# Optimization experiments

Measured on AMD Instinct MI355X. Metric: run time of the kernel, lower is better.

Reference implementation:

```python
import jax, jax.numpy as jnp
import numpy as np

E = 8        # num experts
K = 2        # top-k
H = 1024     # hidden size
F = 3584     # intermediate (ffn) size
B, S = 1, 2048


def setup_inputs() -> dict:
    key = jax.random.key(0)
    ks = jax.random.split(key, 5)
    scale_h = 1.0 / np.sqrt(H)
    scale_f = 1.0 / np.sqrt(F)
    return {
        "hidden_states": jax.random.normal(ks[0], (B, S, H), jnp.float32),
        "gate_w": jax.random.normal(ks[1], (E, H), jnp.float32) * scale_h,  # Linear [out,in]
        "w1": jax.random.normal(ks[2], (E, F, H), jnp.float32) * scale_h,
        "w3": jax.random.normal(ks[3], (E, F, H), jnp.float32) * scale_h,
        "w2": jax.random.normal(ks[4], (E, H, F), jnp.float32) * scale_f,
    }


def reference(hidden_states, gate_w, w1, w3, w2):
    b, s, h = hidden_states.shape
    x = hidden_states.reshape(-1, h)                       # [T,H]
    T = x.shape[0]
    # Router: softmax over experts, top-k, renormalize
    router_logits = x @ gate_w.T                           # [T,E]
    routing_weights = jax.nn.softmax(router_logits.astype(jnp.float32), axis=-1)
    topk_w, topk_idx = jax.lax.top_k(routing_weights, K)   # [T,K]
    topk_w = topk_w / jnp.sum(topk_w, axis=-1, keepdims=True)
    # Per-token, per-expert combine weight (0 for unselected experts) --
    # matches the original mask-and-sum over all experts.
    tok = jnp.arange(T)
    expert_weights = jnp.zeros((T, E), jnp.float32).at[tok[:, None], topk_idx].add(topk_w)  # [T,E]
    # Dense per-expert SiLU-gated MLP over all tokens (as the reference loop does),
    # vectorized across experts.
    g = jnp.einsum("th,efh->etf", x, w1)                   # [E,T,F]
    u = jnp.einsum("th,efh->etf", x, w3)                   # [E,T,F]
    act = jax.nn.silu(g) * u                               # [E,T,F]
    y = jnp.einsum("etf,ehf->eth", act, w2)                # [E,T,H]
    out = jnp.einsum("eth,te->th", y, expert_weights.astype(y.dtype))  # [T,H]
    return out.reshape(b, s, h)
```

## Files before the change

kernel.cpp:

```cpp
#include <hip/hip_runtime.h>
#include <hip/hip_bf16.h>

#define T_TOK 2048
#define HID   1024
#define FF    3584
#define NE    8
#define TOPK  2
#define GRIDY 24

typedef __bf16 bf16x8 __attribute__((ext_vector_type(8)));
typedef float  f32x4  __attribute__((ext_vector_type(4)));
typedef unsigned short u16x8 __attribute__((ext_vector_type(8)));

#define WS_COUNTS   0u
#define WS_OFFSETS  64u
#define WS_TILECNT  128u
#define WS_TLE      256u
#define WS_TLM      512u
#define WS_TOPKI    4096u
#define WS_TOPKW    20480u
#define WS_SLOTPOS  36864u
#define WS_SLOTROW  53248u
#define WS_ROUTETOK 69632u
#define WS_XG       131072u
#define WS_ACT      (WS_XG + 4096u*1024u*2u)
#define WS_Y        (WS_ACT + 4096u*3584u*2u)
#define Y_STRIDE    (4096u*1024u)

static __device__ __forceinline__ unsigned short f2bf(float f) {
    unsigned int u = __builtin_bit_cast(unsigned int, f);
    u += 0x7FFFu + ((u >> 16) & 1u);
    return (unsigned short)(u >> 16);
}
static __device__ __forceinline__ unsigned int cvtpk(float lo, float hi) {
    unsigned int r;
    asm("v_cvt_pk_bf16_f32 %0, %1, %2" : "=v"(r) : "v"(lo), "v"(hi));
    return r;
}

__global__ __launch_bounds__(256) void k_router(
    const float* __restrict__ x, const float* __restrict__ gw,
    int* __restrict__ counts, int* __restrict__ topki,
    float* __restrict__ topkw, int* __restrict__ slotpos)
{
    int t = blockIdx.x * 4 + (threadIdx.x >> 6);
    int l = threadIdx.x & 63;
    const float* xr = x + (size_t)t * HID;
    float acc[NE];
#pragma unroll
    for (int e = 0; e < NE; ++e) acc[e] = 0.f;
#pragma unroll
    for (int i = 0; i < 4; ++i) {
        int h = l * 4 + i * 256;
        float4 xv = *(const float4*)(xr + h);
#pragma unroll
        for (int e = 0; e < NE; ++e) {
            float4 g = *(const float4*)(gw + e * HID + h);
            acc[e] += xv.x * g.x + xv.y * g.y + xv.z * g.z + xv.w * g.w;
        }
    }
#pragma unroll
    for (int e = 0; e < NE; ++e) {
#pragma unroll
        for (int off = 32; off; off >>= 1) acc[e] += __shfl_xor(acc[e], off);
    }
    if (l == 0) {
        float best = -1e30f, second = -1e30f;
        int bi = 0, si = 0;
#pragma unroll
        for (int e = 0; e < NE; ++e) {
            float v = acc[e];
            if (v > best) { second = best; si = bi; best = v; bi = e; }
            else if (v > second) { second = v; si = e; }
        }
        float w0 = 1.f / (1.f + __expf(second - best));
        float w1 = 1.f - w0;
        topki[2 * t] = bi;  topki[2 * t + 1] = si;
        topkw[2 * t] = w0;  topkw[2 * t + 1] = w1;
        slotpos[2 * t]     = atomicAdd(&counts[bi], 1);
        slotpos[2 * t + 1] = atomicAdd(&counts[si], 1);
    }
}

__global__ void k_prefix(const int* __restrict__ counts, int* __restrict__ offsets,
                         int* __restrict__ tle, int* __restrict__ tlm,
                         int* __restrict__ tilecnt) {
    if (threadIdx.x == 0) {
        int o = 0;
#pragma unroll
        for (int e = 0; e < NE; ++e) { offsets[e] = o; o += counts[e]; }
        int n = 0;
        for (int e = 0; e < NE; ++e) {
            int t = (counts[e] + 255) >> 8;
            for (int i = 0; i < t; ++i) { tle[n] = e; tlm[n] = i; ++n; }
        }
        tilecnt[0] = n;
    }
}

__global__ void k_fill(const int* __restrict__ topki, const int* __restrict__ slotpos,
                       const int* __restrict__ offsets, int* __restrict__ routetok,
                       int* __restrict__ slotrow) {
    int j = blockIdx.x * blockDim.x + threadIdx.x;
    if (j >= T_TOK * TOPK) return;
    int e = topki[j];
    int row = offsets[e] + slotpos[j];
    routetok[row] = j >> 1;
    slotrow[j] = row;
}

__global__ void k_gather(const float* __restrict__ x, const int* __restrict__ routetok,
                         unsigned short* __restrict__ xg) {
    int j = blockIdx.x * blockDim.x + threadIdx.x;
    int r = j >> 8;
    int c = (j & 255) * 4;
    int tok = routetok[r];
    float4 v = *(const float4*)(x + (size_t)tok * HID + c);
    ushort4 o;
    o.x = f2bf(v.x); o.y = f2bf(v.y); o.z = f2bf(v.z); o.w = f2bf(v.w);
    int sc = c ^ ((r & 7) << 3);
    *(ushort4*)(xg + (size_t)r * HID + sc) = o;
}

__global__ __launch_bounds__(512, 4) void k_gemm1(
    const unsigned short* __restrict__ xg, const float* __restrict__ w1,
    const float* __restrict__ w3, const int* __restrict__ counts,
    const int* __restrict__ offsets, const int* __restrict__ tle,
    const int* __restrict__ tlm, const int* __restrict__ tilecnt,
    unsigned short* __restrict__ act)
{
    int by = blockIdx.y;
    if (by >= tilecnt[0]) return;
    int e = tle[by];
    int rbase = tlm[by] * 256;
    int cnt = counts[e], obase = offsets[e];
    int fbase = blockIdx.x * 64;

    __shared__ __align__(16) unsigned short lA[256 * 64];
    __shared__ __align__(16) unsigned short lB1[64 * 64];
    __shared__ __align__(16) unsigned short lB3[64 * 64];

    int tid = threadIdx.x;
    const int ra0 = tid >> 3, ca = (tid & 7) * 8;
    const int rb0 = tid >> 4, cb = (tid & 15) * 4;
    const unsigned short* pa[4];
#pragma unroll
    for (int i = 0; i < 4; ++i) {
        int r = obase + rbase + ra0 + 64 * i;
        if (r > 4095) r = 4095;
        pa[i] = xg + (size_t)r * HID + ca;
    }
    const float* w1e = w1 + ((size_t)e * FF + fbase) * HID;
    const float* w3e = w3 + ((size_t)e * FF + fbase) * HID;
    const float* pb1[2];
    const float* pb3[2];
    int wba[2];
#pragma unroll
    for (int i = 0; i < 2; ++i) {
        int row = rb0 + 32 * i;
        pb1[i] = w1e + (size_t)row * HID + cb;
        pb3[i] = w3e + (size_t)row * HID + cb;
        wba[i] = row * 64 + (cb ^ ((row & 7) << 3));
    }

    int lane = tid & 63, wv = tid >> 6, wr = wv >> 1, wc = wv & 1;
    int klane = (lane >> 4) * 8;
    int swzA = (((obase & 7) + (lane & 7)) & 7) << 3;
    int swzB = (lane & 7) << 3;
    f32x4 accg[4][2], accu[4][2];
#pragma unroll
    for (int m = 0; m < 4; ++m)
#pragma unroll
        for (int n = 0; n < 2; ++n) {
            accg[m][n] = (f32x4){0.f, 0.f, 0.f, 0.f};
            accu[m][n] = (f32x4){0.f, 0.f, 0.f, 0.f};
        }

    u16x8 ra[4]; float4 r1[2], r3[2];
#pragma unroll
    for (int i = 0; i < 4; ++i) ra[i] = *(const u16x8*)(pa[i]);
#pragma unroll
    for (int i = 0; i < 2; ++i) { r1[i] = *(const float4*)(pb1[i]); r3[i] = *(const float4*)(pb3[i]); }

    for (int kt = 0; kt < HID / 64; ++kt) {
#pragma unroll
        for (int i = 0; i < 4; ++i)
            *(u16x8*)(lA + (ra0 + 64 * i) * 64 + ca) = ra[i];
#pragma unroll
        for (int i = 0; i < 2; ++i) {
            uint2 p;
            p.x = cvtpk(r1[i].x, r1[i].y); p.y = cvtpk(r1[i].z, r1[i].w);
            *(uint2*)(lB1 + wba[i]) = p;
            p.x = cvtpk(r3[i].x, r3[i].y); p.y = cvtpk(r3[i].z, r3[i].w);
            *(uint2*)(lB3 + wba[i]) = p;
        }
        __syncthreads();
        if (kt < HID / 64 - 1) {
            int kof = (kt + 1) * 64;
#pragma unroll
            for (int i = 0; i < 4; ++i) ra[i] = *(const u16x8*)(pa[i] + kof);
#pragma unroll
            for (int i = 0; i < 2; ++i) {
                r1[i] = *(const float4*)(pb1[i] + kof);
                r3[i] = *(const float4*)(pb3[i] + kof);
            }
        }
#pragma unroll
        for (int kk = 0; kk < 64; kk += 32) {
            int kc = kk + klane;
            int kA = kc ^ swzA, kB = kc ^ swzB;
            bf16x8 a[4], b1[2], b3[2];
#pragma unroll
            for (int m = 0; m < 4; ++m)
                a[m] = *(const bf16x8*)(lA + (wr * 64 + m * 16 + (lane & 15)) * 64 + kA);
#pragma unroll
            for (int n = 0; n < 2; ++n) {
                b1[n] = *(const bf16x8*)(lB1 + (wc * 32 + n * 16 + (lane & 15)) * 64 + kB);
                b3[n] = *(const bf16x8*)(lB3 + (wc * 32 + n * 16 + (lane & 15)) * 64 + kB);
            }
#pragma unroll
            for (int m = 0; m < 4; ++m)
#pragma unroll
                for (int n = 0; n < 2; ++n) {
                    accg[m][n] = __builtin_amdgcn_mfma_f32_16x16x32_bf16(a[m], b1[n], accg[m][n], 0, 0, 0);
                    accu[m][n] = __builtin_amdgcn_mfma_f32_16x16x32_bf16(a[m], b3[n], accu[m][n], 0, 0, 0);
                }
        }
        __syncthreads();
    }

#pragma unroll
    for (int m = 0; m < 4; ++m)
#pragma unroll
        for (int n = 0; n < 2; ++n)
#pragma unroll
            for (int r = 0; r < 4; ++r) {
                int lr = wr * 64 + m * 16 + (lane >> 4) * 4 + r;
                if (rbase + lr < cnt) {
                    float g = accg[m][n][r], u = accu[m][n][r];
                    float s = g / (1.f + __expf(-g));
                    int row = obase + rbase + lr;
                    int col = fbase + wc * 32 + n * 16 + (lane & 15);
                    int scol = col ^ ((row & 7) << 3);
                    act[(size_t)row * FF + scol] = f2bf(s * u);
                }
            }
}

__global__ __launch_bounds__(512, 4) void k_gemm2(
    const unsigned short* __restrict__ act, const float* __restrict__ w2,
    const int* __restrict__ counts, const int* __restrict__ offsets,
    const int* __restrict__ tle, const int* __restrict__ tlm,
    const int* __restrict__ tilecnt, float* __restrict__ y, int ks)
{
    int by = blockIdx.y;
    if (by >= tilecnt[0]) return;
    int e = tle[by];
    int rbase = tlm[by] * 256;
    int cnt = counts[e], obase = offsets[e];
    int hbase = blockIdx.x * 128;
    int z = blockIdx.z;
    const int KTOT = FF / 64;
    int per = (KTOT + ks - 1) / ks;
    int kt0 = z * per;
    int ktn = (KTOT < kt0 + per ? KTOT : kt0 + per) - kt0;
    int kb0 = kt0 * 64;

    __shared__ __align__(16) unsigned short lA[256 * 64];
    __shared__ __align__(16) unsigned short lB[128 * 64];

    int tid = threadIdx.x;
    const int ra0 = tid >> 3, ca = (tid & 7) * 8;
    const unsigned short* pa[4];
#pragma unroll
    for (int i = 0; i < 4; ++i) {
        int r = obase + rbase + ra0 + 64 * i;
        if (r > 4095) r = 4095;
        pa[i] = act + (size_t)r * FF + kb0 + ca;
    }
    int hr = tid >> 2, cbf = (tid & 3) * 16;
    const float* pb = w2 + ((size_t)e * HID + hbase + hr) * FF + kb0 + cbf;
    int wbb[2];
#pragma unroll
    for (int g = 0; g < 2; ++g)
        wbb[g] = hr * 64 + ((cbf + g * 8) ^ ((hr & 7) << 3));

    int lane = tid & 63, wv = tid >> 6;
    int wr = wv & 3, wc = wv >> 2;
    int klane = (lane >> 4) * 8;
    int swzA = (((obase & 7) + (lane & 7)) & 7) << 3;
    int swzB = (lane & 7) << 3;
    f32x4 acc[4][4];
#pragma unroll
    for (int m = 0; m < 4; ++m)
#pragma unroll
        for (int n = 0; n < 4; ++n) acc[m][n] = (f32x4){0.f, 0.f, 0.f, 0.f};

    u16x8 ra[4]; float4 rw[4];
#pragma unroll
    for (int i = 0; i < 4; ++i) ra[i] = *(const u16x8*)(pa[i]);
#pragma unroll
    for (int j = 0; j < 4; ++j) rw[j] = *(const float4*)(pb + 4 * j);

    for (int kt = 0; kt < ktn; ++kt) {
#pragma unroll
        for (int i = 0; i < 4; ++i)
            *(u16x8*)(lA + (ra0 + 64 * i) * 64 + ca) = ra[i];
#pragma unroll
        for (int g = 0; g < 2; ++g) {
            uint4 q;
            q.x = cvtpk(rw[2 * g].x, rw[2 * g].y);
            q.y = cvtpk(rw[2 * g].z, rw[2 * g].w);
            q.z = cvtpk(rw[2 * g + 1].x, rw[2 * g + 1].y);
            q.w = cvtpk(rw[2 * g + 1].z, rw[2 * g + 1].w);
            *(uint4*)(lB + wbb[g]) = q;
        }
        __syncthreads();
        if (kt < ktn - 1) {
            int kof = (kt + 1) * 64;
#pragma unroll
            for (int i = 0; i < 4; ++i) ra[i] = *(const u16x8*)(pa[i] + kof);
#pragma unroll
            for (int j = 0; j < 4; ++j) rw[j] = *(const float4*)(pb + kof + 4 * j);
        }
#pragma unroll
        for (int kk = 0; kk < 64; kk += 32) {
            int kc = kk + klane;
            int kA = kc ^ swzA, kB = kc ^ swzB;
            bf16x8 a[4], b[4];
#pragma unroll
            for (int m = 0; m < 4; ++m)
                a[m] = *(const bf16x8*)(lA + (wr * 64 + m * 16 + (lane & 15)) * 64 + kA);
#pragma unroll
            for (int n = 0; n < 4; ++n)
                b[n] = *(const bf16x8*)(lB + (wc * 64 + n * 16 + (lane & 15)) * 64 + kB);
#pragma unroll
            for (int m = 0; m < 4; ++m)
#pragma unroll
                for (int n = 0; n < 4; ++n)
                    acc[m][n] = __builtin_amdgcn_mfma_f32_16x16x32_bf16(a[m], b[n], acc[m][n], 0, 0, 0);
        }
        __syncthreads();
    }

    float* yz = y + (size_t)z * Y_STRIDE;
#pragma unroll
    for (int m = 0; m < 4; ++m)
#pragma unroll
        for (int n = 0; n < 4; ++n)
#pragma unroll
            for (int r = 0; r < 4; ++r) {
                int lr = wr * 64 + m * 16 + (lane >> 4) * 4 + r;
                if (rbase + lr < cnt) {
                    int col = hbase + wc * 64 + n * 16 + (lane & 15);
                    yz[(size_t)(obase + rbase + lr) * HID + col] = acc[m][n][r];
                }
            }
}

__global__ void k_combine(const float* __restrict__ y, const int* __restrict__ slotrow,
                          const float* __restrict__ topkw, float* __restrict__ out, int ks) {
    int j = blockIdx.x * blockDim.x + threadIdx.x;
    int t = j >> 8, c = j & 255;
    int r0 = slotrow[2 * t], r1 = slotrow[2 * t + 1];
    float w0 = topkw[2 * t], w1 = topkw[2 * t + 1];
    float4 a = {0.f, 0.f, 0.f, 0.f}, b = {0.f, 0.f, 0.f, 0.f};
    for (int z = 0; z < ks; ++z) {
        const float4* yz = (const float4*)(y + (size_t)z * Y_STRIDE);
        float4 av = yz[(size_t)r0 * 256 + c];
        float4 bv = yz[(size_t)r1 * 256 + c];
        a.x += av.x; a.y += av.y; a.z += av.z; a.w += av.w;
        b.x += bv.x; b.y += bv.y; b.z += bv.z; b.w += bv.w;
    }
    float4 o;
    o.x = w0 * a.x + w1 * b.x;
    o.y = w0 * a.y + w1 * b.y;
    o.z = w0 * a.z + w1 * b.z;
    o.w = w0 * a.w + w1 * b.w;
    ((float4*)out)[j] = o;
}

extern "C" void kernel_launch(void* const* d_in, const int* in_sizes, int n_in,
                              void* d_out, int out_size, void* d_ws, size_t ws_size,
                              hipStream_t stream) {
    const float* x  = (const float*)d_in[0];
    const float* gw = (const float*)d_in[1];
    const float* w1 = (const float*)d_in[2];
    const float* w3 = (const float*)d_in[3];
    const float* w2 = (const float*)d_in[4];
    float* out = (float*)d_out;

    char* ws = (char*)d_ws;
    int*   counts   = (int*)(ws + WS_COUNTS);
    int*   offsets  = (int*)(ws + WS_OFFSETS);
    int*   tilecnt  = (int*)(ws + WS_TILECNT);
    int*   tle      = (int*)(ws + WS_TLE);
    int*   tlm      = (int*)(ws + WS_TLM);
    int*   topki    = (int*)(ws + WS_TOPKI);
    float* topkw    = (float*)(ws + WS_TOPKW);
    int*   slotpos  = (int*)(ws + WS_SLOTPOS);
    int*   slotrow  = (int*)(ws + WS_SLOTROW);
    int*   routetok = (int*)(ws + WS_ROUTETOK);
    unsigned short* xg   = (unsigned short*)(ws + WS_XG);
    unsigned short* actb = (unsigned short*)(ws + WS_ACT);
    float* yb = (float*)(ws + WS_Y);

    size_t ybytes = (size_t)Y_STRIDE * 4;
    int ks = (ws_size >= (size_t)WS_Y + 3 * ybytes) ? 3 : 2;

    hipMemsetAsync(counts, 0, 64, stream);
    k_router<<<T_TOK / 4, 256, 0, stream>>>(x, gw, counts, topki, topkw, slotpos);
    k_prefix<<<1, 64, 0, stream>>>(counts, offsets, tle, tlm, tilecnt);
    k_fill<<<16, 256, 0, stream>>>(topki, slotpos, offsets, routetok, slotrow);
    k_gather<<<4096, 256, 0, stream>>>(x, routetok, xg);
    k_gemm1<<<dim3(FF / 64, GRIDY, 1), 512, 0, stream>>>(xg, w1, w3, counts, offsets, tle, tlm, tilecnt, actb);
    k_gemm2<<<dim3(HID / 128, GRIDY, ks), 512, 0, stream>>>(actb, w2, counts, offsets, tle, tlm, tilecnt, yb, ks);
    k_combine<<<2048, 256, 0, stream>>>(yb, slotrow, topkw, out, ks);
}
```

Before: 264.4 us.

## Enlarge gemm1 row tile to 512 tokens with 1024-thread blocks

```diff
diff --git a/kernel.cpp b/kernel.cpp
--- a/kernel.cpp
+++ b/kernel.cpp
@@ -6,7 +6,8 @@
 #define FF    3584
 #define NE    8
 #define TOPK  2
-#define GRIDY 24
+#define GRIDY1 16
+#define GRIDY2 24
 
 typedef __bf16 bf16x8 __attribute__((ext_vector_type(8)));
 typedef float  f32x4  __attribute__((ext_vector_type(4)));
@@ -15,8 +16,10 @@
 #define WS_COUNTS   0u
 #define WS_OFFSETS  64u
 #define WS_TILECNT  128u
-#define WS_TLE      256u
-#define WS_TLM      512u
+#define WS_TLE1     256u
+#define WS_TLM1     512u
+#define WS_TLE2     768u
+#define WS_TLM2     1024u
 #define WS_TOPKI    4096u
 #define WS_TOPKW    20480u
 #define WS_SLOTPOS  36864u
@@ -83,18 +86,21 @@
 }
 
 __global__ void k_prefix(const int* __restrict__ counts, int* __restrict__ offsets,
-                         int* __restrict__ tle, int* __restrict__ tlm,
+                         int* __restrict__ tl1e, int* __restrict__ tl1m,
+                         int* __restrict__ tl2e, int* __restrict__ tl2m,
                          int* __restrict__ tilecnt) {
     if (threadIdx.x == 0) {
         int o = 0;
 #pragma unroll
         for (int e = 0; e < NE; ++e) { offsets[e] = o; o += counts[e]; }
-        int n = 0;
+        int n1 = 0, n2 = 0;
         for (int e = 0; e < NE; ++e) {
-            int t = (counts[e] + 255) >> 8;
-            for (int i = 0; i < t; ++i) { tle[n] = e; tlm[n] = i; ++n; }
-        }
-        tilecnt[0] = n;
+            int t1 = (counts[e] + 511) >> 9;
+            for (int i = 0; i < t1; ++i) { tl1e[n1] = e; tl1m[n1] = i; ++n1; }
+            int t2 = (counts[e] + 255) >> 8;
+            for (int i = 0; i < t2; ++i) { tl2e[n2] = e; tl2m[n2] = i; ++n2; }
+        }
+        tilecnt[0] = n1; tilecnt[1] = n2;
     }
 }
 
@@ -122,7 +128,7 @@
     *(ushort4*)(xg + (size_t)r * HID + sc) = o;
 }
 
-__global__ __launch_bounds__(512, 4) void k_gemm1(
+__global__ __launch_bounds__(1024, 2) void k_gemm1(
     const unsigned short* __restrict__ xg, const float* __restrict__ w1,
     const float* __restrict__ w3, const int* __restrict__ counts,
     const int* __restrict__ offsets, const int* __restrict__ tle,
@@ -132,11 +138,11 @@
     int by = blockIdx.y;
     if (by >= tilecnt[0]) return;
     int e = tle[by];
-    int rbase = tlm[by] * 256;
+    int rbase = tlm[by] * 512;
     int cnt = counts[e], obase = offsets[e];
     int fbase = blockIdx.x * 64;
 
-    __shared__ __align__(16) unsigned short lA[256 * 64];
+    __shared__ __align__(16) unsigned short lA[512 * 64];
     __shared__ __align__(16) unsigned short lB1[64 * 64];
     __shared__ __align__(16) unsigned short lB3[64 * 64];
 
@@ -146,24 +152,16 @@
     const unsigned short* pa[4];
 #pragma unroll
     for (int i = 0; i < 4; ++i) {
-        int r = obase + rbase + ra0 + 64 * i;
+        int r = obase + rbase + ra0 + 128 * i;
         if (r > 4095) r = 4095;
         pa[i] = xg + (size_t)r * HID + ca;
     }
-    const float* w1e = w1 + ((size_t)e * FF + fbase) * HID;
-    const float* w3e = w3 + ((size_t)e * FF + fbase) * HID;
-    const float* pb1[2];
-    const float* pb3[2];
-    int wba[2];
-#pragma unroll
-    for (int i = 0; i < 2; ++i) {
-        int row = rb0 + 32 * i;
-        pb1[i] = w1e + (size_t)row * HID + cb;
-        pb3[i] = w3e + (size_t)row * HID + cb;
-        wba[i] = row * 64 + (cb ^ ((row & 7) << 3));
-    }
-
-    int lane = tid & 63, wv = tid >> 6, wr = wv >> 1, wc = wv & 1;
+    const float* pb1 = w1 + ((size_t)e * FF + fbase + rb0) * HID + cb;
+    const float* pb3 = w3 + ((size_t)e * FF + fbase + rb0) * HID + cb;
+    int wba = rb0 * 64 + (cb ^ ((rb0 & 7) << 3));
+
+    int lane = tid & 63, wv = tid >> 6;
+    int wr = wv >> 1, wc = wv & 1;
     int klane = (lane >> 4) * 8;
     int swzA = (((obase & 7) + (lane & 7)) & 7) << 3;
     int swzB = (lane & 7) << 3;
@@ -176,34 +174,30 @@
             accu[m][n] = (f32x4){0.f, 0.f, 0.f, 0.f};
         }
 
-    u16x8 ra[4]; float4 r1[2], r3[2];
+    u16x8 ra[4]; float4 r1, r3;
 #pragma unroll
     for (int i = 0; i < 4; ++i) ra[i] = *(const u16x8*)(pa[i]);
-#pragma unroll
-    for (int i = 0; i < 2; ++i) { r1[i] = *(const float4*)(pb1[i]); r3[i] = *(const float4*)(pb3[i]); }
+    r1 = *(const float4*)(pb1);
+    r3 = *(const float4*)(pb3);
 
     for (int kt = 0; kt < HID / 64; ++kt) {
 #pragma unroll
         for (int i = 0; i < 4; ++i)
-            *(u16x8*)(lA + (ra0 + 64 * i) * 64 + ca) = ra[i];
-#pragma unroll
-        for (int i = 0; i < 2; ++i) {
+            *(u16x8*)(lA + (ra0 + 128 * i) * 64 + ca) = ra[i];
+        {
             uint2 p;
-            p.x = cvtpk(r1[i].x, r1[i].y); p.y = cvtpk(r1[i].z, r1[i].w);
-            *(uint2*)(lB1 + wba[i]) = p;
-            p.x = cvtpk(r3[i].x, r3[i].y); p.y = cvtpk(r3[i].z, r3[i].w);
-            *(uint2*)(lB3 + wba[i]) = p;
+            p.x = cvtpk(r1.x, r1.y); p.y = cvtpk(r1.z, r1.w);
+            *(uint2*)(lB1 + wba) = p;
+            p.x = cvtpk(r3.x, r3.y); p.y = cvtpk(r3.z, r3.w);
+            *(uint2*)(lB3 + wba) = p;
         }
         __syncthreads();
         if (kt < HID / 64 - 1) {
             int kof = (kt + 1) * 64;
 #pragma unroll
             for (int i = 0; i < 4; ++i) ra[i] = *(const u16x8*)(pa[i] + kof);
-#pragma unroll
-            for (int i = 0; i < 2; ++i) {
-                r1[i] = *(const float4*)(pb1[i] + kof);
-                r3[i] = *(const float4*)(pb3[i] + kof);
-            }
+            r1 = *(const float4*)(pb1 + kof);
+            r3 = *(const float4*)(pb3 + kof);
         }
 #pragma unroll
         for (int kk = 0; kk < 64; kk += 32) {
@@ -254,7 +248,7 @@
     const int* __restrict__ tilecnt, float* __restrict__ y, int ks)
 {
     int by = blockIdx.y;
-    if (by >= tilecnt[0]) return;
+    if (by >= tilecnt[1]) return;
     int e = tle[by];
     int rbase = tlm[by] * 256;
     int cnt = counts[e], obase = offsets[e];
@@ -394,8 +388,10 @@
     int*   counts   = (int*)(ws + WS_COUNTS);
     int*   offsets  = (int*)(ws + WS_OFFSETS);
     int*   tilecnt  = (int*)(ws + WS_TILECNT);
-    int*   tle      = (int*)(ws + WS_TLE);
-    int*   tlm      = (int*)(ws + WS_TLM);
+    int*   tl1e     = (int*)(ws + WS_TLE1);
+    int*   tl1m     = (int*)(ws + WS_TLM1);
+    int*   tl2e     = (int*)(ws + WS_TLE2);
+    int*   tl2m     = (int*)(ws + WS_TLM2);
     int*   topki    = (int*)(ws + WS_TOPKI);
     float* topkw    = (float*)(ws + WS_TOPKW);
     int*   slotpos  = (int*)(ws + WS_SLOTPOS);
@@ -410,10 +406,10 @@
 
     hipMemsetAsync(counts, 0, 64, stream);
     k_router<<<T_TOK / 4, 256, 0, stream>>>(x, gw, counts, topki, topkw, slotpos);
-    k_prefix<<<1, 64, 0, stream>>>(counts, offsets, tle, tlm, tilecnt);
+    k_prefix<<<1, 64, 0, stream>>>(counts, offsets, tl1e, tl1m, tl2e, tl2m, tilecnt);
     k_fill<<<16, 256, 0, stream>>>(topki, slotpos, offsets, routetok, slotrow);
     k_gather<<<4096, 256, 0, stream>>>(x, routetok, xg);
-    k_gemm1<<<dim3(FF / 64, GRIDY, 1), 512, 0, stream>>>(xg, w1, w3, counts, offsets, tle, tlm, tilecnt, actb);
-    k_gemm2<<<dim3(HID / 128, GRIDY, ks), 512, 0, stream>>>(actb, w2, counts, offsets, tle, tlm, tilecnt, yb, ks);
+    k_gemm1<<<dim3(FF / 64, GRIDY1, 1), 1024, 0, stream>>>(xg, w1, w3, counts, offsets, tl1e, tl1m, tilecnt, actb);
+    k_gemm2<<<dim3(HID / 128, GRIDY2, ks), 512, 0, stream>>>(actb, w2, counts, offsets, tl2e, tl2m, tilecnt, yb, ks);
     k_combine<<<2048, 256, 0, stream>>>(yb, slotrow, topkw, out, ks);
 }
```

Result: slower. 287.8 us (+8.9%).

## Fuse fill and gather kernels; remap GEMM grids to XCD-aware 1D order

Applied to the files above, without the earlier changes.

```diff
diff --git a/kernel.cpp b/kernel.cpp
--- a/kernel.cpp
+++ b/kernel.cpp
@@ -98,28 +98,26 @@
     }
 }
 
-__global__ void k_fill(const int* __restrict__ topki, const int* __restrict__ slotpos,
-                       const int* __restrict__ offsets, int* __restrict__ routetok,
-                       int* __restrict__ slotrow) {
-    int j = blockIdx.x * blockDim.x + threadIdx.x;
-    if (j >= T_TOK * TOPK) return;
+__global__ __launch_bounds__(256) void k_fillgather(
+    const float* __restrict__ x, const int* __restrict__ topki,
+    const int* __restrict__ slotpos, const int* __restrict__ offsets,
+    int* __restrict__ routetok, int* __restrict__ slotrow,
+    unsigned short* __restrict__ xg)
+{
+    int j = blockIdx.x;
     int e = topki[j];
     int row = offsets[e] + slotpos[j];
-    routetok[row] = j >> 1;
-    slotrow[j] = row;
-}
-
-__global__ void k_gather(const float* __restrict__ x, const int* __restrict__ routetok,
-                         unsigned short* __restrict__ xg) {
-    int j = blockIdx.x * blockDim.x + threadIdx.x;
-    int r = j >> 8;
-    int c = (j & 255) * 4;
-    int tok = routetok[r];
+    int tok = j >> 1;
+    if (threadIdx.x == 0) {
+        routetok[row] = tok;
+        slotrow[j] = row;
+    }
+    int c = threadIdx.x * 4;
     float4 v = *(const float4*)(x + (size_t)tok * HID + c);
     ushort4 o;
     o.x = f2bf(v.x); o.y = f2bf(v.y); o.z = f2bf(v.z); o.w = f2bf(v.w);
-    int sc = c ^ ((r & 7) << 3);
-    *(ushort4*)(xg + (size_t)r * HID + sc) = o;
+    int sc = c ^ ((row & 7) << 3);
+    *(ushort4*)(xg + (size_t)row * HID + sc) = o;
 }
 
 __global__ __launch_bounds__(512, 4) void k_gemm1(
@@ -129,12 +127,15 @@
     const int* __restrict__ tlm, const int* __restrict__ tilecnt,
     unsigned short* __restrict__ act)
 {
-    int by = blockIdx.y;
+    int d = blockIdx.x;
+    int xcd = d & 7, s = d >> 3;
+    int fx = s % 56, byg = s / 56;
+    int by = xcd + 8 * byg;
     if (by >= tilecnt[0]) return;
     int e = tle[by];
     int rbase = tlm[by] * 256;
     int cnt = counts[e], obase = offsets[e];
-    int fbase = blockIdx.x * 64;
+    int fbase = fx * 64;
 
     __shared__ __align__(16) unsigned short lA[256 * 64];
     __shared__ __align__(16) unsigned short lB1[64 * 64];
@@ -253,13 +254,18 @@
     const int* __restrict__ tle, const int* __restrict__ tlm,
     const int* __restrict__ tilecnt, float* __restrict__ y, int ks)
 {
-    int by = blockIdx.y;
+    int d = blockIdx.x;
+    int xcd = d & 7, s = d >> 3;
+    int hx = s & 7, s2 = s >> 3;
+    int z = s2 % 3;
+    int byg = s2 / 3;
+    int by = xcd + 8 * byg;
     if (by >= tilecnt[0]) return;
+    if (z >= ks) return;
     int e = tle[by];
     int rbase = tlm[by] * 256;
     int cnt = counts[e], obase = offsets[e];
-    int hbase = blockIdx.x * 128;
-    int z = blockIdx.z;
+    int hbase = hx * 128;
     const int KTOT = FF / 64;
     int per = (KTOT + ks - 1) / ks;
     int kt0 = z * per;
@@ -411,9 +417,8 @@
     hipMemsetAsync(counts, 0, 64, stream);
     k_router<<<T_TOK / 4, 256, 0, stream>>>(x, gw, counts, topki, topkw, slotpos);
     k_prefix<<<1, 64, 0, stream>>>(counts, offsets, tle, tlm, tilecnt);
-    k_fill<<<16, 256, 0, stream>>>(topki, slotpos, offsets, routetok, slotrow);
-    k_gather<<<4096, 256, 0, stream>>>(x, routetok, xg);
-    k_gemm1<<<dim3(FF / 64, GRIDY, 1), 512, 0, stream>>>(xg, w1, w3, counts, offsets, tle, tlm, tilecnt, actb);
-    k_gemm2<<<dim3(HID / 128, GRIDY, ks), 512, 0, stream>>>(actb, w2, counts, offsets, tle, tlm, tilecnt, yb, ks);
+    k_fillgather<<<T_TOK * TOPK, 256, 0, stream>>>(x, topki, slotpos, offsets, routetok, slotrow, xg);
+    k_gemm1<<<56 * GRIDY, 512, 0, stream>>>(xg, w1, w3, counts, offsets, tle, tlm, tilecnt, actb);
+    k_gemm2<<<8 * 3 * GRIDY, 512, 0, stream>>>(actb, w2, counts, offsets, tle, tlm, tilecnt, yb, ks);
     k_combine<<<2048, 256, 0, stream>>>(yb, slotrow, topkw, out, ks);
 }
```

After: 318.7 us. 20.5% more time.
